# Kernel optimization log

Measured on AMD Instinct MI355X. Metric: run time of the kernel, lower is better.

The kernel has to match this reference:

```python
import jax, jax.numpy as jnp
import numpy as np

N, D, C, K = 16384, 128, 10, 16
EPS = float(np.finfo(np.float32).eps)
LOG2PI = float(np.log(2.0 * np.pi))


def setup_inputs() -> dict:
    key = jax.random.key(0)
    ks = jax.random.split(key, 8)
    X = jax.random.normal(ks[0], (N, D), dtype=jnp.float32)
    y = jax.random.randint(ks[1], (N,), 0, C, dtype=jnp.int32)
    responsibilities = jax.random.uniform(ks[2], (C, N, K), dtype=jnp.float32)
    mu = jax.random.normal(ks[3], (C, K, D), dtype=jnp.float32)
    # lower < mu < upper so the truncation normalizer is positive (as after gmm_initialisation)
    lower = mu - 1.0 + 0.1 * jax.random.normal(ks[4], (C, K, D), dtype=jnp.float32)
    upper = mu + 1.0 + 0.1 * jax.random.normal(ks[5], (C, K, D), dtype=jnp.float32)
    sigma = jnp.abs(jax.random.normal(ks[6], (C, K, D), dtype=jnp.float32))
    logits_k = jax.random.normal(ks[7], (C, K), dtype=jnp.float32)
    eta = jnp.float32(0.0)  # model initializes eta = 0.0 (non-trainable)
    return {"X": X, "y": y, "responsibilities": responsibilities, "mu": mu,
            "lower": lower, "upper": upper, "sigma": sigma,
            "logits_k": logits_k, "eta": eta}


def _stgma_loss(X, y, responsibilities, mu, lower, upper, sigma, logits_k, eta):
    # scale = eps + softplus(sigma), shape [C, K, D]
    scale = EPS + jax.nn.softplus(sigma)
    # normalizing constant per (class, component): prod_d [Phi(up) - Phi(lo)] + eps
    ndtr = jax.scipy.special.ndtr
    z = ndtr((upper - mu) / scale) - ndtr((lower - mu) / scale)       # [C, K, D]
    log_norm = jnp.log(jnp.prod(z, axis=-1) + EPS)                    # [C, K]
    log_cat = jax.nn.log_softmax(logits_k, axis=-1)                   # [C, K]

    # gather per-sample class parameters: [N, K, D]
    mu_y, lo_y, up_y, sc_y = mu[y], lower[y], upper[y], scale[y]
    xk = X[:, None, :]                                                # [N, 1, D]

    # soft truncation margins: sum_d -softplus(-eta * (x - lower)) etc.
    lp_low = -jnp.sum(jax.nn.softplus(-eta * (xk - lo_y)), axis=-1)   # [N, K]
    lp_up = -jnp.sum(jax.nn.softplus(-eta * (up_y - xk)), axis=-1)    # [N, K]

    # independent diagonal Normal log prob per component
    zd = (xk - mu_y) / sc_y
    comp_lp = jnp.sum(-0.5 * zd * zd - jnp.log(sc_y), axis=-1) - 0.5 * D * LOG2PI  # [N, K]

    log_pdf = log_cat[y] - log_norm[y] + lp_low + lp_up + comp_lp     # [N, K]

    # responsibilities for each sample from its own class
    resp = responsibilities[y, jnp.arange(N)]                         # [N, K]
    weighted = resp * log_pdf                                         # [N, K]

    # per-class reduce_mean over the class's samples and components, then -sum
    onehot = (y[:, None] == jnp.arange(C)[None, :]).astype(weighted.dtype)  # [N, C]
    class_sums = jnp.einsum('nk,nc->c', weighted, onehot)             # [C]
    counts = jnp.sum(onehot, axis=0) * K                              # [C]
    return -jnp.sum(class_sums / counts)


def reference(X, y, responsibilities, mu, lower, upper, sigma, logits_k, eta):
    return _stgma_loss(X, y, responsibilities, mu, lower, upper, sigma, logits_k, eta)
```

## Files before the change

kernel.cpp:

```cpp
#include <hip/hip_runtime.h>
#include <math.h>

#define N_PTS 16384
#define D_DIM 128
#define C_CLS 10
#define K_MIX 16

constexpr float EPSF   = 1.1920928955078125e-07f;
constexpr float LOG2PI = 1.8378770664093453f;
constexpr float LN2F   = 0.6931471805599453f;

__device__ __forceinline__ float softplusf(float x) {
    if (x > 20.f)  return x;
    if (x < -20.f) return expf(x);
    return log1pf(expf(x));
}
__device__ __forceinline__ float ndtrf(float x) {
    return 0.5f * erfcf(-x * 0.70710678118654752440f);
}

__global__ __launch_bounds__(64) void k_params(
    const float* __restrict__ mu, const float* __restrict__ lower,
    const float* __restrict__ upper, const float* __restrict__ sigma,
    float* __restrict__ muT, float* __restrict__ isT,
    float* __restrict__ loT, float* __restrict__ upT,
    float* __restrict__ Ack) {
    int b = blockIdx.x;
    int c = b / K_MIX, k = b % K_MIX;
    int lane = threadIdx.x;
    float ls_sum = 0.f;
    float zprod  = 1.f;
    #pragma unroll
    for (int half = 0; half < 2; ++half) {
        int d  = lane + 64 * half;
        int gi = (c * K_MIX + k) * D_DIM + d;
        float m  = mu[gi], lo = lower[gi], up = upper[gi], sg = sigma[gi];
        float sc = EPSF + softplusf(sg);
        float is = 1.f / sc;
        int ti = c * (D_DIM * K_MIX) + d * K_MIX + k;
        muT[ti] = m; isT[ti] = is; loT[ti] = lo; upT[ti] = up;
        ls_sum += logf(sc);
        float z = ndtrf((up - m) * is) - ndtrf((lo - m) * is);
        zprod *= z;
    }
    #pragma unroll
    for (int off = 1; off < 64; off <<= 1) {
        ls_sum += __shfl_xor(ls_sum, off);
        zprod  *= __shfl_xor(zprod, off);
    }
    if (lane == 0) {
        float log_norm = logf(zprod + EPSF);
        Ack[b] = -log_norm - ls_sum - 0.5f * (float)D_DIM * LOG2PI;
    }
}

__global__ __launch_bounds__(256) void k_const(
    const float* __restrict__ logits, const int* __restrict__ y,
    const float* __restrict__ Ack,
    float* __restrict__ const_ck, int* __restrict__ counts) {
    __shared__ int hist[C_CLS];
    int t = threadIdx.x;
    if (t < C_CLS) hist[t] = 0;
    __syncthreads();
    for (int i = t; i < N_PTS; i += 256) atomicAdd(&hist[y[i]], 1);
    __syncthreads();
    if (t < C_CLS) {
        int c = t;
        counts[c] = hist[c];
        float mx = -1e30f;
        for (int k = 0; k < K_MIX; ++k) mx = fmaxf(mx, logits[c * K_MIX + k]);
        float se = 0.f;
        for (int k = 0; k < K_MIX; ++k) se += expf(logits[c * K_MIX + k] - mx);
        float lse = mx + logf(se);
        for (int k = 0; k < K_MIX; ++k)
            const_ck[c * K_MIX + k] = logits[c * K_MIX + k] - lse + Ack[c * K_MIX + k];
    }
}

__global__ __launch_bounds__(256) void k_main(
    const float* __restrict__ X, const int* __restrict__ y,
    const float* __restrict__ resp,
    const float* __restrict__ muT, const float* __restrict__ isT,
    const float* __restrict__ loT, const float* __restrict__ upT,
    const float* __restrict__ const_ck, const int* __restrict__ counts,
    const float* __restrict__ etap, float* __restrict__ blockPartials) {
    __shared__ float xs[16][132];
    __shared__ float sums[16];
    int t  = threadIdx.x;
    int n0 = blockIdx.x * 16;

    #pragma unroll
    for (int i = 0; i < 2; ++i) {
        int j  = t * 2 + i;
        int r  = j >> 5, c4 = j & 31;
        float4 v = *reinterpret_cast<const float4*>(X + (size_t)(n0 + r) * D_DIM + c4 * 4);
        xs[r][c4 * 4 + 0] = v.x; xs[r][c4 * 4 + 1] = v.y;
        xs[r][c4 * 4 + 2] = v.z; xs[r][c4 * 4 + 3] = v.w;
    }
    __syncthreads();

    int k  = t & 15;
    int nl = (t >> 4) & 3;
    int w  = t >> 6;
    int n_local = w * 4 + nl;
    int n  = n0 + n_local;
    int c  = y[n];

    const float* mp = muT + (size_t)c * (D_DIM * K_MIX) + k;
    const float* sp = isT + (size_t)c * (D_DIM * K_MIX) + k;

    float acc = 0.f;
    #pragma unroll 4
    for (int d = 0; d < D_DIM; ++d) {
        float x  = xs[n_local][d];
        float zd = (x - mp[d * K_MIX]) * sp[d * K_MIX];
        acc = fmaf(zd, zd, acc);
    }

    float eta = etap[0];
    float lp;
    if (eta == 0.f) {
        lp = -2.f * (float)D_DIM * LN2F;
    } else {
        lp = 0.f;
        const float* lo = loT + (size_t)c * (D_DIM * K_MIX) + k;
        const float* up = upT + (size_t)c * (D_DIM * K_MIX) + k;
        for (int d = 0; d < D_DIM; ++d) {
            float x = xs[n_local][d];
            lp -= softplusf(-eta * (x - lo[d * K_MIX]))
                + softplusf(-eta * (up[d * K_MIX] - x));
        }
    }

    float r_ = resp[((size_t)c * N_PTS + n) * K_MIX + k];
    float v  = r_ * (const_ck[c * K_MIX + k] + lp - 0.5f * acc);
    v *= 1.f / ((float)counts[c] * (float)K_MIX);

    v += __shfl_xor(v, 1);
    v += __shfl_xor(v, 2);
    v += __shfl_xor(v, 4);
    v += __shfl_xor(v, 8);
    if (k == 0) sums[n_local] = v;
    __syncthreads();
    if (t == 0) {
        float s = 0.f;
        #pragma unroll
        for (int i = 0; i < 16; ++i) s += sums[i];
        blockPartials[blockIdx.x] = s;
    }
}

__global__ __launch_bounds__(256) void k_final(
    const float* __restrict__ blockPartials, float* __restrict__ out) {
    __shared__ float red[256];
    int t = threadIdx.x;
    float s = 0.f;
    for (int i = t; i < 1024; i += 256) s += blockPartials[i];
    red[t] = s;
    __syncthreads();
    for (int off = 128; off > 0; off >>= 1) {
        if (t < off) red[t] += red[t + off];
        __syncthreads();
    }
    if (t == 0) out[0] = -red[0];
}

extern "C" void kernel_launch(void* const* d_in, const int* in_sizes, int n_in,
                              void* d_out, int out_size, void* d_ws, size_t ws_size,
                              hipStream_t stream) {
    const float* X      = (const float*)d_in[0];
    const int*   y      = (const int*)  d_in[1];
    const float* resp   = (const float*)d_in[2];
    const float* mu     = (const float*)d_in[3];
    const float* lower  = (const float*)d_in[4];
    const float* upper  = (const float*)d_in[5];
    const float* sigma  = (const float*)d_in[6];
    const float* logits = (const float*)d_in[7];
    const float* eta    = (const float*)d_in[8];
    float* out = (float*)d_out;

    char* ws = (char*)d_ws;
    size_t off = 0;
    auto alloc = [&](size_t bytes) {
        void* p = ws + off;
        off += (bytes + 255) & ~size_t(255);
        return p;
    };
    const size_t PARAM = (size_t)C_CLS * D_DIM * K_MIX * sizeof(float);
    float* muT      = (float*)alloc(PARAM);
    float* isT      = (float*)alloc(PARAM);
    float* loT      = (float*)alloc(PARAM);
    float* upT      = (float*)alloc(PARAM);
    float* Ack      = (float*)alloc(C_CLS * K_MIX * sizeof(float));
    float* const_ck = (float*)alloc(C_CLS * K_MIX * sizeof(float));
    int*   counts   = (int*)  alloc(C_CLS * sizeof(int));
    float* partials = (float*)alloc((N_PTS / 16) * sizeof(float));

    k_params<<<C_CLS * K_MIX, 64, 0, stream>>>(mu, lower, upper, sigma,
                                               muT, isT, loT, upT, Ack);
    k_const<<<1, 256, 0, stream>>>(logits, y, Ack, const_ck, counts);
    k_main<<<N_PTS / 16, 256, 0, stream>>>(X, y, resp, muT, isT, loT, upT,
                                           const_ck, counts, eta, partials);
    k_final<<<1, 256, 0, stream>>>(partials, out);
}
```

Baseline: 35.02 us.

## Sort samples by class and keep per-class parameters in registers

```diff
diff --git a/kernel.cpp b/kernel.cpp
--- a/kernel.cpp
+++ b/kernel.cpp
@@ -5,6 +5,8 @@
 #define D_DIM 128
 #define C_CLS 10
 #define K_MIX 16
+#define HIST_BLOCKS 64
+#define MAIN_BPC 32
 
 constexpr float EPSF   = 1.1920928955078125e-07f;
 constexpr float LOG2PI = 1.8378770664093453f;
@@ -19,143 +21,205 @@
     return 0.5f * erfcf(-x * 0.70710678118654752440f);
 }
 
-__global__ __launch_bounds__(64) void k_params(
+__global__ __launch_bounds__(256) void k_prep(
     const float* __restrict__ mu, const float* __restrict__ lower,
     const float* __restrict__ upper, const float* __restrict__ sigma,
-    float* __restrict__ muT, float* __restrict__ isT,
-    float* __restrict__ loT, float* __restrict__ upT,
-    float* __restrict__ Ack) {
+    const int* __restrict__ y,
+    float2* __restrict__ abT, float* __restrict__ loT, float* __restrict__ upT,
+    float* __restrict__ Ack, int* __restrict__ blockCnt) {
+    int b = blockIdx.x, t = threadIdx.x;
+    if (b < C_CLS * K_MIX) {
+        int c = b / K_MIX, k = b % K_MIX;
+        __shared__ float rs0[256], rs1[256], rp[256];
+        float logsc = 0.f, mu2 = 0.f, zz = 1.f;
+        if (t < D_DIM) {
+            int gi = b * D_DIM + t;
+            float m = mu[gi], lo = lower[gi], up = upper[gi], sg = sigma[gi];
+            float sc = EPSF + softplusf(sg);
+            float is = 1.f / sc;
+            int ti = (c * D_DIM + t) * K_MIX + k;
+            abT[ti] = make_float2(is * is, 2.f * m * is * is);
+            loT[ti] = lo; upT[ti] = up;
+            logsc = logf(sc);
+            mu2   = m * m * is * is;
+            zz    = ndtrf((up - m) * is) - ndtrf((lo - m) * is);
+        }
+        rs0[t] = logsc; rs1[t] = mu2; rp[t] = zz;
+        __syncthreads();
+        for (int off = 128; off > 0; off >>= 1) {
+            if (t < off) { rs0[t] += rs0[t+off]; rs1[t] += rs1[t+off]; rp[t] *= rp[t+off]; }
+            __syncthreads();
+        }
+        if (t == 0) {
+            float log_norm = logf(rp[0] + EPSF);
+            Ack[b] = -log_norm - rs0[0] - 0.5f * (float)D_DIM * LOG2PI - 0.5f * rs1[0];
+        }
+    } else {
+        int h = b - C_CLS * K_MIX;
+        __shared__ int hist[C_CLS];
+        if (t < C_CLS) hist[t] = 0;
+        __syncthreads();
+        int c = y[h * 256 + t];
+        int lane = t & 63;
+        for (int cc = 0; cc < C_CLS; ++cc) {
+            unsigned long long m = __ballot(c == cc);
+            if (lane == 0 && m) atomicAdd(&hist[cc], __popcll(m));
+        }
+        __syncthreads();
+        if (t < C_CLS) blockCnt[h * C_CLS + t] = hist[t];
+    }
+}
+
+__global__ __launch_bounds__(256) void k_scatter(
+    const int* __restrict__ y, const int* __restrict__ blockCnt,
+    const float* __restrict__ logits, const float* __restrict__ Ack,
+    int* __restrict__ idxSorted, int* __restrict__ classOff,
+    float* __restrict__ invden, float* __restrict__ const_ck) {
+    __shared__ int sCnt[HIST_BLOCKS * C_CLS];
+    __shared__ int sClassOff[C_CLS + 1];
+    __shared__ int myOff[C_CLS];
+    __shared__ int wcnt[4][C_CLS];
+    __shared__ int wbase[4][C_CLS];
+    int h = blockIdx.x, t = threadIdx.x;
+    for (int i = t; i < HIST_BLOCKS * C_CLS; i += 256) sCnt[i] = blockCnt[i];
+    __syncthreads();
+    if (t == 0) {
+        int acc = 0;
+        for (int c = 0; c < C_CLS; ++c) {
+            sClassOff[c] = acc;
+            int s = 0;
+            for (int hh = 0; hh < HIST_BLOCKS; ++hh) s += sCnt[hh * C_CLS + c];
+            acc += s;
+        }
+        sClassOff[C_CLS] = acc;
+    }
+    __syncthreads();
+    if (t < C_CLS) {
+        int s = sClassOff[t];
+        for (int hh = 0; hh < h; ++hh) s += sCnt[hh * C_CLS + t];
+        myOff[t] = s;
+    }
+    __syncthreads();
+    int n = h * 256 + t;
+    int c = y[n];
+    int w = t >> 6, lane = t & 63;
+    int rank = 0;
+    for (int cc = 0; cc < C_CLS; ++cc) {
+        unsigned long long m = __ballot(c == cc);
+        if (c == cc) rank = __popcll(m & ((1ull << lane) - 1ull));
+        if (lane == 0) wcnt[w][cc] = __popcll(m);
+    }
+    __syncthreads();
+    if (t < 4 * C_CLS) {
+        int ww = t / C_CLS, cc = t % C_CLS;
+        int s = myOff[cc];
+        for (int w2 = 0; w2 < ww; ++w2) s += wcnt[w2][cc];
+        wbase[ww][cc] = s;
+    }
+    __syncthreads();
+    idxSorted[wbase[w][c] + rank] = n;
+
+    if (h == 0) {
+        __shared__ float lse[C_CLS];
+        if (t < C_CLS) {
+            float mx = -1e30f;
+            for (int k = 0; k < K_MIX; ++k) mx = fmaxf(mx, logits[t * K_MIX + k]);
+            float se = 0.f;
+            for (int k = 0; k < K_MIX; ++k) se += expf(logits[t * K_MIX + k] - mx);
+            lse[t] = mx + logf(se);
+            int cnt = sClassOff[t + 1] - sClassOff[t];
+            invden[t] = (cnt > 0) ? 1.f / ((float)cnt * (float)K_MIX) : 0.f;
+        }
+        if (t < C_CLS + 1) classOff[t] = sClassOff[t];
+        __syncthreads();
+        if (t < C_CLS * K_MIX) const_ck[t] = logits[t] - lse[t / K_MIX] + Ack[t];
+    }
+}
+
+__global__ __launch_bounds__(256) void k_main(
+    const float* __restrict__ X, const float* __restrict__ resp,
+    const float2* __restrict__ abT, const float* __restrict__ loT,
+    const float* __restrict__ upT, const float* __restrict__ const_ck,
+    const int* __restrict__ classOff, const float* __restrict__ invden,
+    const int* __restrict__ idxSorted, const float* __restrict__ etap,
+    float* __restrict__ partials) {
     int b = blockIdx.x;
-    int c = b / K_MIX, k = b % K_MIX;
-    int lane = threadIdx.x;
-    float ls_sum = 0.f;
-    float zprod  = 1.f;
+    int c = b / MAIN_BPC, j = b % MAIN_BPC;
+    int t = threadIdx.x;
+    int w = t >> 6, lane = t & 63;
+    int k = lane & 15, dc = lane >> 4;
+    const int d0 = dc * 32;
+
+    float a_[32], b_[32];
+    const float2* ab = abT + (size_t)c * D_DIM * K_MIX + k;
     #pragma unroll
-    for (int half = 0; half < 2; ++half) {
-        int d  = lane + 64 * half;
-        int gi = (c * K_MIX + k) * D_DIM + d;
-        float m  = mu[gi], lo = lower[gi], up = upper[gi], sg = sigma[gi];
-        float sc = EPSF + softplusf(sg);
-        float is = 1.f / sc;
-        int ti = c * (D_DIM * K_MIX) + d * K_MIX + k;
-        muT[ti] = m; isT[ti] = is; loT[ti] = lo; upT[ti] = up;
-        ls_sum += logf(sc);
-        float z = ndtrf((up - m) * is) - ndtrf((lo - m) * is);
-        zprod *= z;
-    }
-    #pragma unroll
-    for (int off = 1; off < 64; off <<= 1) {
-        ls_sum += __shfl_xor(ls_sum, off);
-        zprod  *= __shfl_xor(zprod, off);
-    }
-    if (lane == 0) {
-        float log_norm = logf(zprod + EPSF);
-        Ack[b] = -log_norm - ls_sum - 0.5f * (float)D_DIM * LOG2PI;
-    }
-}
-
-__global__ __launch_bounds__(256) void k_const(
-    const float* __restrict__ logits, const int* __restrict__ y,
-    const float* __restrict__ Ack,
-    float* __restrict__ const_ck, int* __restrict__ counts) {
-    __shared__ int hist[C_CLS];
-    int t = threadIdx.x;
-    if (t < C_CLS) hist[t] = 0;
-    __syncthreads();
-    for (int i = t; i < N_PTS; i += 256) atomicAdd(&hist[y[i]], 1);
-    __syncthreads();
-    if (t < C_CLS) {
-        int c = t;
-        counts[c] = hist[c];
-        float mx = -1e30f;
-        for (int k = 0; k < K_MIX; ++k) mx = fmaxf(mx, logits[c * K_MIX + k]);
-        float se = 0.f;
-        for (int k = 0; k < K_MIX; ++k) se += expf(logits[c * K_MIX + k] - mx);
-        float lse = mx + logf(se);
-        for (int k = 0; k < K_MIX; ++k)
-            const_ck[c * K_MIX + k] = logits[c * K_MIX + k] - lse + Ack[c * K_MIX + k];
-    }
-}
-
-__global__ __launch_bounds__(256) void k_main(
-    const float* __restrict__ X, const int* __restrict__ y,
-    const float* __restrict__ resp,
-    const float* __restrict__ muT, const float* __restrict__ isT,
-    const float* __restrict__ loT, const float* __restrict__ upT,
-    const float* __restrict__ const_ck, const int* __restrict__ counts,
-    const float* __restrict__ etap, float* __restrict__ blockPartials) {
-    __shared__ float xs[16][132];
-    __shared__ float sums[16];
-    int t  = threadIdx.x;
-    int n0 = blockIdx.x * 16;
-
-    #pragma unroll
-    for (int i = 0; i < 2; ++i) {
-        int j  = t * 2 + i;
-        int r  = j >> 5, c4 = j & 31;
-        float4 v = *reinterpret_cast<const float4*>(X + (size_t)(n0 + r) * D_DIM + c4 * 4);
-        xs[r][c4 * 4 + 0] = v.x; xs[r][c4 * 4 + 1] = v.y;
-        xs[r][c4 * 4 + 2] = v.z; xs[r][c4 * 4 + 3] = v.w;
-    }
-    __syncthreads();
-
-    int k  = t & 15;
-    int nl = (t >> 4) & 3;
-    int w  = t >> 6;
-    int n_local = w * 4 + nl;
-    int n  = n0 + n_local;
-    int c  = y[n];
-
-    const float* mp = muT + (size_t)c * (D_DIM * K_MIX) + k;
-    const float* sp = isT + (size_t)c * (D_DIM * K_MIX) + k;
-
-    float acc = 0.f;
-    #pragma unroll 4
-    for (int d = 0; d < D_DIM; ++d) {
-        float x  = xs[n_local][d];
-        float zd = (x - mp[d * K_MIX]) * sp[d * K_MIX];
-        acc = fmaf(zd, zd, acc);
-    }
-
+    for (int i = 0; i < 32; ++i) {
+        float2 v = ab[(size_t)(d0 + i) * K_MIX];
+        a_[i] = v.x; b_[i] = v.y;
+    }
+    float ck  = const_ck[c * K_MIX + k];
     float eta = etap[0];
-    float lp;
-    if (eta == 0.f) {
-        lp = -2.f * (float)D_DIM * LN2F;
-    } else {
-        lp = 0.f;
-        const float* lo = loT + (size_t)c * (D_DIM * K_MIX) + k;
-        const float* up = upT + (size_t)c * (D_DIM * K_MIX) + k;
-        for (int d = 0; d < D_DIM; ++d) {
-            float x = xs[n_local][d];
-            lp -= softplusf(-eta * (x - lo[d * K_MIX]))
-                + softplusf(-eta * (up[d * K_MIX] - x));
-        }
-    }
-
-    float r_ = resp[((size_t)c * N_PTS + n) * K_MIX + k];
-    float v  = r_ * (const_ck[c * K_MIX + k] + lp - 0.5f * acc);
-    v *= 1.f / ((float)counts[c] * (float)K_MIX);
-
-    v += __shfl_xor(v, 1);
-    v += __shfl_xor(v, 2);
-    v += __shfl_xor(v, 4);
-    v += __shfl_xor(v, 8);
-    if (k == 0) sums[n_local] = v;
-    __syncthreads();
-    if (t == 0) {
-        float s = 0.f;
-        #pragma unroll
-        for (int i = 0; i < 16; ++i) s += sums[i];
-        blockPartials[blockIdx.x] = s;
-    }
+    float inv = invden[c];
+    int off = classOff[c];
+    int cnt = classOff[c + 1] - off;
+    const float lpconst = -2.f * (float)D_DIM * LN2F;
+
+    float wsum = 0.f;
+    for (int p = j * 4 + w; p < cnt; p += MAIN_BPC * 4) {
+        int n = idxSorted[off + p];
+        const float* xr = X + (size_t)n * D_DIM + d0;
+        float acc = 0.f, lp = lpconst;
+        if (eta == 0.f) {
+            #pragma unroll
+            for (int i4 = 0; i4 < 8; ++i4) {
+                float4 xv = *reinterpret_cast<const float4*>(xr + i4 * 4);
+                acc = fmaf(xv.x, fmaf(a_[i4*4+0], xv.x, -b_[i4*4+0]), acc);
+                acc = fmaf(xv.y, fmaf(a_[i4*4+1], xv.y, -b_[i4*4+1]), acc);
+                acc = fmaf(xv.z, fmaf(a_[i4*4+2], xv.z, -b_[i4*4+2]), acc);
+                acc = fmaf(xv.w, fmaf(a_[i4*4+3], xv.w, -b_[i4*4+3]), acc);
+            }
+            acc += __shfl_xor(acc, 16);
+            acc += __shfl_xor(acc, 32);
+        } else {
+            float lpp = 0.f;
+            const float* lo = loT + (size_t)c * D_DIM * K_MIX + k;
+            const float* up = upT + (size_t)c * D_DIM * K_MIX + k;
+            #pragma unroll
+            for (int i4 = 0; i4 < 8; ++i4) {
+                float4 xv = *reinterpret_cast<const float4*>(xr + i4 * 4);
+                float xs4[4] = {xv.x, xv.y, xv.z, xv.w};
+                #pragma unroll
+                for (int q = 0; q < 4; ++q) {
+                    int i = i4 * 4 + q;
+                    float x = xs4[q];
+                    acc = fmaf(x, fmaf(a_[i], x, -b_[i]), acc);
+                    float lov = lo[(size_t)(d0 + i) * K_MIX];
+                    float upv = up[(size_t)(d0 + i) * K_MIX];
+                    lpp -= softplusf(-eta * (x - lov)) + softplusf(-eta * (upv - x));
+                }
+            }
+            acc += __shfl_xor(acc, 16); acc += __shfl_xor(acc, 32);
+            lpp += __shfl_xor(lpp, 16); lpp += __shfl_xor(lpp, 32);
+            lp = lpp;
+        }
+        float r = resp[((size_t)c * N_PTS + n) * K_MIX + k];
+        float v = r * (ck + lp - 0.5f * acc) * inv;
+        v += __shfl_xor(v, 1); v += __shfl_xor(v, 2);
+        v += __shfl_xor(v, 4); v += __shfl_xor(v, 8);
+        wsum += v;
+    }
+    __shared__ float ws[4];
+    if (lane == 0) ws[w] = wsum;
+    __syncthreads();
+    if (t == 0) partials[b] = ws[0] + ws[1] + ws[2] + ws[3];
 }
 
 __global__ __launch_bounds__(256) void k_final(
-    const float* __restrict__ blockPartials, float* __restrict__ out) {
+    const float* __restrict__ partials, float* __restrict__ out) {
     __shared__ float red[256];
     int t = threadIdx.x;
     float s = 0.f;
-    for (int i = t; i < 1024; i += 256) s += blockPartials[i];
+    for (int i = t; i < C_CLS * MAIN_BPC; i += 256) s += partials[i];
     red[t] = s;
     __syncthreads();
     for (int off = 128; off > 0; off >>= 1) {
@@ -186,20 +250,23 @@
         off += (bytes + 255) & ~size_t(255);
         return p;
     };
-    const size_t PARAM = (size_t)C_CLS * D_DIM * K_MIX * sizeof(float);
-    float* muT      = (float*)alloc(PARAM);
-    float* isT      = (float*)alloc(PARAM);
-    float* loT      = (float*)alloc(PARAM);
-    float* upT      = (float*)alloc(PARAM);
-    float* Ack      = (float*)alloc(C_CLS * K_MIX * sizeof(float));
-    float* const_ck = (float*)alloc(C_CLS * K_MIX * sizeof(float));
-    int*   counts   = (int*)  alloc(C_CLS * sizeof(int));
-    float* partials = (float*)alloc((N_PTS / 16) * sizeof(float));
-
-    k_params<<<C_CLS * K_MIX, 64, 0, stream>>>(mu, lower, upper, sigma,
-                                               muT, isT, loT, upT, Ack);
-    k_const<<<1, 256, 0, stream>>>(logits, y, Ack, const_ck, counts);
-    k_main<<<N_PTS / 16, 256, 0, stream>>>(X, y, resp, muT, isT, loT, upT,
-                                           const_ck, counts, eta, partials);
+    const size_t PE = (size_t)C_CLS * D_DIM * K_MIX;
+    float2* abT      = (float2*)alloc(PE * sizeof(float2));
+    float*  loT      = (float*) alloc(PE * sizeof(float));
+    float*  upT      = (float*) alloc(PE * sizeof(float));
+    float*  Ack      = (float*) alloc(C_CLS * K_MIX * sizeof(float));
+    float*  const_ck = (float*) alloc(C_CLS * K_MIX * sizeof(float));
+    int*    blockCnt = (int*)   alloc(HIST_BLOCKS * C_CLS * sizeof(int));
+    int*    idxSorted= (int*)   alloc(N_PTS * sizeof(int));
+    int*    classOff = (int*)   alloc((C_CLS + 1) * sizeof(int));
+    float*  invden   = (float*) alloc(C_CLS * sizeof(float));
+    float*  partials = (float*) alloc(C_CLS * MAIN_BPC * sizeof(float));
+
+    k_prep<<<C_CLS * K_MIX + HIST_BLOCKS, 256, 0, stream>>>(
+        mu, lower, upper, sigma, y, abT, loT, upT, Ack, blockCnt);
+    k_scatter<<<HIST_BLOCKS, 256, 0, stream>>>(
+        y, blockCnt, logits, Ack, idxSorted, classOff, invden, const_ck);
+    k_main<<<C_CLS * MAIN_BPC, 256, 0, stream>>>(
+        X, resp, abT, loT, upT, const_ck, classOff, invden, idxSorted, eta, partials);
     k_final<<<1, 256, 0, stream>>>(partials, out);
 }
```

New measurement: 34.53 us. About the same (-1.4%).

## Fuse param prep into class-partitioned main kernel with register-resident expanded quadratic

Applied to the files above, without the earlier changes.

```diff
diff --git a/kernel.cpp b/kernel.cpp
--- a/kernel.cpp
+++ b/kernel.cpp
@@ -5,6 +5,9 @@
 #define D_DIM 128
 #define C_CLS 10
 #define K_MIX 16
+#define BPC   51
+#define GRID  (C_CLS * BPC)
+#define NCHUNK (N_PTS / 64)
 
 constexpr float EPSF   = 1.1920928955078125e-07f;
 constexpr float LOG2PI = 1.8378770664093453f;
@@ -19,150 +22,189 @@
     return 0.5f * erfcf(-x * 0.70710678118654752440f);
 }
 
-__global__ __launch_bounds__(64) void k_params(
+__global__ __launch_bounds__(256, 2) void k_main(
+    const float* __restrict__ X, const int* __restrict__ y,
+    const float* __restrict__ resp,
     const float* __restrict__ mu, const float* __restrict__ lower,
     const float* __restrict__ upper, const float* __restrict__ sigma,
-    float* __restrict__ muT, float* __restrict__ isT,
-    float* __restrict__ loT, float* __restrict__ upT,
-    float* __restrict__ Ack) {
-    int b = blockIdx.x;
-    int c = b / K_MIX, k = b % K_MIX;
-    int lane = threadIdx.x;
-    float ls_sum = 0.f;
-    float zprod  = 1.f;
+    const float* __restrict__ etap,
+    float* __restrict__ Ack, float* __restrict__ partials1,
+    float* __restrict__ partials2, int* __restrict__ countB) {
+    const int b = blockIdx.x, t = threadIdx.x;
+    const int w = t >> 6, lane = t & 63;
+    const int c = b / BPC, j = b % BPC;
+    const int k = lane & 15, dc = lane >> 4;
+    const int d0 = dc * 32;
+
+    __shared__ float zW[4][16];
+    __shared__ float sWsum[4];
+    __shared__ float sRk[4][16];
+    __shared__ int   sCntW[4];
+
+    const size_t pbase = ((size_t)(c * K_MIX + k)) * D_DIM + d0;
+    float a_[32], b_[32];
+    float logsc = 0.f, mu2 = 0.f;
     #pragma unroll
-    for (int half = 0; half < 2; ++half) {
-        int d  = lane + 64 * half;
-        int gi = (c * K_MIX + k) * D_DIM + d;
-        float m  = mu[gi], lo = lower[gi], up = upper[gi], sg = sigma[gi];
-        float sc = EPSF + softplusf(sg);
-        float is = 1.f / sc;
-        int ti = c * (D_DIM * K_MIX) + d * K_MIX + k;
-        muT[ti] = m; isT[ti] = is; loT[ti] = lo; upT[ti] = up;
-        ls_sum += logf(sc);
-        float z = ndtrf((up - m) * is) - ndtrf((lo - m) * is);
-        zprod *= z;
-    }
-    #pragma unroll
-    for (int off = 1; off < 64; off <<= 1) {
-        ls_sum += __shfl_xor(ls_sum, off);
-        zprod  *= __shfl_xor(zprod, off);
-    }
-    if (lane == 0) {
-        float log_norm = logf(zprod + EPSF);
-        Ack[b] = -log_norm - ls_sum - 0.5f * (float)D_DIM * LOG2PI;
-    }
-}
-
-__global__ __launch_bounds__(256) void k_const(
-    const float* __restrict__ logits, const int* __restrict__ y,
-    const float* __restrict__ Ack,
-    float* __restrict__ const_ck, int* __restrict__ counts) {
-    __shared__ int hist[C_CLS];
-    int t = threadIdx.x;
-    if (t < C_CLS) hist[t] = 0;
-    __syncthreads();
-    for (int i = t; i < N_PTS; i += 256) atomicAdd(&hist[y[i]], 1);
-    __syncthreads();
-    if (t < C_CLS) {
-        int c = t;
-        counts[c] = hist[c];
-        float mx = -1e30f;
-        for (int k = 0; k < K_MIX; ++k) mx = fmaxf(mx, logits[c * K_MIX + k]);
-        float se = 0.f;
-        for (int k = 0; k < K_MIX; ++k) se += expf(logits[c * K_MIX + k] - mx);
-        float lse = mx + logf(se);
-        for (int k = 0; k < K_MIX; ++k)
-            const_ck[c * K_MIX + k] = logits[c * K_MIX + k] - lse + Ack[c * K_MIX + k];
-    }
-}
-
-__global__ __launch_bounds__(256) void k_main(
-    const float* __restrict__ X, const int* __restrict__ y,
-    const float* __restrict__ resp,
-    const float* __restrict__ muT, const float* __restrict__ isT,
-    const float* __restrict__ loT, const float* __restrict__ upT,
-    const float* __restrict__ const_ck, const int* __restrict__ counts,
-    const float* __restrict__ etap, float* __restrict__ blockPartials) {
-    __shared__ float xs[16][132];
-    __shared__ float sums[16];
-    int t  = threadIdx.x;
-    int n0 = blockIdx.x * 16;
-
-    #pragma unroll
-    for (int i = 0; i < 2; ++i) {
-        int j  = t * 2 + i;
-        int r  = j >> 5, c4 = j & 31;
-        float4 v = *reinterpret_cast<const float4*>(X + (size_t)(n0 + r) * D_DIM + c4 * 4);
-        xs[r][c4 * 4 + 0] = v.x; xs[r][c4 * 4 + 1] = v.y;
-        xs[r][c4 * 4 + 2] = v.z; xs[r][c4 * 4 + 3] = v.w;
-    }
-    __syncthreads();
-
-    int k  = t & 15;
-    int nl = (t >> 4) & 3;
-    int w  = t >> 6;
-    int n_local = w * 4 + nl;
-    int n  = n0 + n_local;
-    int c  = y[n];
-
-    const float* mp = muT + (size_t)c * (D_DIM * K_MIX) + k;
-    const float* sp = isT + (size_t)c * (D_DIM * K_MIX) + k;
-
-    float acc = 0.f;
-    #pragma unroll 4
-    for (int d = 0; d < D_DIM; ++d) {
-        float x  = xs[n_local][d];
-        float zd = (x - mp[d * K_MIX]) * sp[d * K_MIX];
-        acc = fmaf(zd, zd, acc);
-    }
-
-    float eta = etap[0];
-    float lp;
-    if (eta == 0.f) {
-        lp = -2.f * (float)D_DIM * LN2F;
-    } else {
-        lp = 0.f;
-        const float* lo = loT + (size_t)c * (D_DIM * K_MIX) + k;
-        const float* up = upT + (size_t)c * (D_DIM * K_MIX) + k;
-        for (int d = 0; d < D_DIM; ++d) {
-            float x = xs[n_local][d];
-            lp -= softplusf(-eta * (x - lo[d * K_MIX]))
-                + softplusf(-eta * (up[d * K_MIX] - x));
-        }
-    }
-
-    float r_ = resp[((size_t)c * N_PTS + n) * K_MIX + k];
-    float v  = r_ * (const_ck[c * K_MIX + k] + lp - 0.5f * acc);
-    v *= 1.f / ((float)counts[c] * (float)K_MIX);
-
-    v += __shfl_xor(v, 1);
-    v += __shfl_xor(v, 2);
-    v += __shfl_xor(v, 4);
-    v += __shfl_xor(v, 8);
-    if (k == 0) sums[n_local] = v;
+    for (int i4 = 0; i4 < 8; ++i4) {
+        float4 mv = *reinterpret_cast<const float4*>(mu    + pbase + i4 * 4);
+        float4 sv = *reinterpret_cast<const float4*>(sigma + pbase + i4 * 4);
+        float m4[4] = {mv.x, mv.y, mv.z, mv.w};
+        float s4[4] = {sv.x, sv.y, sv.z, sv.w};
+        #pragma unroll
+        for (int q = 0; q < 4; ++q) {
+            int i = i4 * 4 + q;
+            float sc = EPSF + softplusf(s4[q]);
+            float is = 1.f / sc;
+            a_[i] = is * is;
+            b_[i] = 2.f * m4[q] * is * is;
+            logsc += logf(sc);
+            mu2   += m4[q] * m4[q] * is * is;
+        }
+    }
+
+    if (j == 0) {
+        float zp = 1.f;
+        const size_t zbase = pbase + w * 8;
+        #pragma unroll
+        for (int i4 = 0; i4 < 2; ++i4) {
+            float4 mv = *reinterpret_cast<const float4*>(mu    + zbase + i4 * 4);
+            float4 sv = *reinterpret_cast<const float4*>(sigma + zbase + i4 * 4);
+            float4 lv = *reinterpret_cast<const float4*>(lower + zbase + i4 * 4);
+            float4 uv = *reinterpret_cast<const float4*>(upper + zbase + i4 * 4);
+            float m4[4] = {mv.x, mv.y, mv.z, mv.w};
+            float s4[4] = {sv.x, sv.y, sv.z, sv.w};
+            float l4[4] = {lv.x, lv.y, lv.z, lv.w};
+            float u4[4] = {uv.x, uv.y, uv.z, uv.w};
+            #pragma unroll
+            for (int q = 0; q < 4; ++q) {
+                float sc = EPSF + softplusf(s4[q]);
+                float is = 1.f / sc;
+                zp *= ndtrf((u4[q] - m4[q]) * is) - ndtrf((l4[q] - m4[q]) * is);
+            }
+        }
+        zp *= __shfl_xor(zp, 16);
+        zp *= __shfl_xor(zp, 32);
+        if (lane < 16) zW[w][lane] = zp;
+    }
+    float logscF = logsc + 0.f, mu2F = mu2 + 0.f;
+    logscF += __shfl_xor(logscF, 16); logscF += __shfl_xor(logscF, 32);
+    mu2F   += __shfl_xor(mu2F, 16);   mu2F   += __shfl_xor(mu2F, 32);
+    if (j == 0) {
+        __syncthreads();
+        if (w == 0 && lane < 16) {
+            float zp = zW[0][lane] * zW[1][lane] * zW[2][lane] * zW[3][lane];
+            Ack[c * K_MIX + lane] = -logf(zp + EPSF) - logscF
+                                  - 0.5f * (float)D_DIM * LOG2PI - 0.5f * mu2F;
+        }
+    }
+
+    const float eta = etap[0];
+    const float lpconst = -2.f * (float)D_DIM * LN2F;
+    float wsum = 0.f, rk = 0.f;
+    int myCount = 0;
+
+    for (int q = j * 4 + w; q < NCHUNK; q += BPC * 4) {
+        int n0 = q * 64;
+        int yv = y[n0 + lane];
+        unsigned long long m = __ballot(yv == c);
+        myCount += __popcll(m);
+        while (m) {
+            int s = __builtin_ctzll(m);
+            m &= m - 1;
+            int n = n0 + s;
+            const float* xr = X + (size_t)n * D_DIM + d0;
+            float acc = 0.f, lp = lpconst;
+            #pragma unroll
+            for (int i4 = 0; i4 < 8; ++i4) {
+                float4 xv = *reinterpret_cast<const float4*>(xr + i4 * 4);
+                acc = fmaf(xv.x, fmaf(a_[i4*4+0], xv.x, -b_[i4*4+0]), acc);
+                acc = fmaf(xv.y, fmaf(a_[i4*4+1], xv.y, -b_[i4*4+1]), acc);
+                acc = fmaf(xv.z, fmaf(a_[i4*4+2], xv.z, -b_[i4*4+2]), acc);
+                acc = fmaf(xv.w, fmaf(a_[i4*4+3], xv.w, -b_[i4*4+3]), acc);
+            }
+            if (eta != 0.f) {
+                float lpp = 0.f;
+                #pragma unroll
+                for (int i4 = 0; i4 < 8; ++i4) {
+                    float4 xv = *reinterpret_cast<const float4*>(xr + i4 * 4);
+                    float4 lv = *reinterpret_cast<const float4*>(lower + pbase + i4 * 4);
+                    float4 uv = *reinterpret_cast<const float4*>(upper + pbase + i4 * 4);
+                    float x4[4] = {xv.x, xv.y, xv.z, xv.w};
+                    float l4[4] = {lv.x, lv.y, lv.z, lv.w};
+                    float u4[4] = {uv.x, uv.y, uv.z, uv.w};
+                    #pragma unroll
+                    for (int qq = 0; qq < 4; ++qq)
+                        lpp -= softplusf(-eta * (x4[qq] - l4[qq]))
+                             + softplusf(-eta * (u4[qq] - x4[qq]));
+                }
+                lpp += __shfl_xor(lpp, 16);
+                lpp += __shfl_xor(lpp, 32);
+                lp = lpp;
+            }
+            acc += __shfl_xor(acc, 16);
+            acc += __shfl_xor(acc, 32);
+            float r = resp[((size_t)c * N_PTS + n) * K_MIX + k];
+            rk += r;
+            float v = r * fmaf(-0.5f, acc, lp);
+            v += __shfl_xor(v, 1); v += __shfl_xor(v, 2);
+            v += __shfl_xor(v, 4); v += __shfl_xor(v, 8);
+            wsum += v;
+        }
+    }
+
+    if (lane == 0) { sWsum[w] = wsum; sCntW[w] = myCount; }
+    if (lane < 16) sRk[w][lane] = rk;
     __syncthreads();
     if (t == 0) {
+        partials1[b] = sWsum[0] + sWsum[1] + sWsum[2] + sWsum[3];
+        countB[b]    = sCntW[0] + sCntW[1] + sCntW[2] + sCntW[3];
+    }
+    if (t < K_MIX)
+        partials2[b * K_MIX + t] = sRk[0][t] + sRk[1][t] + sRk[2][t] + sRk[3][t];
+}
+
+__global__ __launch_bounds__(256) void k_final(
+    const float* __restrict__ logits, const float* __restrict__ Ack,
+    const float* __restrict__ partials1, const float* __restrict__ partials2,
+    const int* __restrict__ countB, float* __restrict__ out) {
+    __shared__ float sS1[C_CLS];
+    __shared__ int   sCnt[C_CLS];
+    __shared__ float sLse[C_CLS];
+    __shared__ float sR[C_CLS * K_MIX];
+    int t = threadIdx.x;
+    if (t < C_CLS) {
+        float s = 0.f; int cn = 0;
+        for (int jj = 0; jj < BPC; ++jj) {
+            s  += partials1[t * BPC + jj];
+            cn += countB[t * BPC + jj];
+        }
+        sS1[t] = s; sCnt[t] = cn;
+        float mx = -1e30f;
+        for (int k = 0; k < K_MIX; ++k) mx = fmaxf(mx, logits[t * K_MIX + k]);
+        float se = 0.f;
+        for (int k = 0; k < K_MIX; ++k) se += expf(logits[t * K_MIX + k] - mx);
+        sLse[t] = mx + logf(se);
+    }
+    if (t < C_CLS * K_MIX) {
+        int c = t / K_MIX, k = t % K_MIX;
         float s = 0.f;
-        #pragma unroll
-        for (int i = 0; i < 16; ++i) s += sums[i];
-        blockPartials[blockIdx.x] = s;
-    }
-}
-
-__global__ __launch_bounds__(256) void k_final(
-    const float* __restrict__ blockPartials, float* __restrict__ out) {
-    __shared__ float red[256];
-    int t = threadIdx.x;
-    float s = 0.f;
-    for (int i = t; i < 1024; i += 256) s += blockPartials[i];
-    red[t] = s;
+        for (int jj = 0; jj < BPC; ++jj)
+            s += partials2[((size_t)(c * BPC + jj)) * K_MIX + k];
+        sR[t] = s;
+    }
     __syncthreads();
-    for (int off = 128; off > 0; off >>= 1) {
-        if (t < off) red[t] += red[t + off];
-        __syncthreads();
-    }
-    if (t == 0) out[0] = -red[0];
+    if (t == 0) {
+        float loss = 0.f;
+        for (int c = 0; c < C_CLS; ++c) {
+            float cs = sS1[c];
+            for (int k = 0; k < K_MIX; ++k)
+                cs += sR[c * K_MIX + k]
+                    * (logits[c * K_MIX + k] - sLse[c] + Ack[c * K_MIX + k]);
+            float den = (float)sCnt[c] * (float)K_MIX;
+            if (sCnt[c] > 0) loss += cs / den;
+        }
+        out[0] = -loss;
+    }
 }
 
 extern "C" void kernel_launch(void* const* d_in, const int* in_sizes, int n_in,
@@ -186,20 +228,12 @@
         off += (bytes + 255) & ~size_t(255);
         return p;
     };
-    const size_t PARAM = (size_t)C_CLS * D_DIM * K_MIX * sizeof(float);
-    float* muT      = (float*)alloc(PARAM);
-    float* isT      = (float*)alloc(PARAM);
-    float* loT      = (float*)alloc(PARAM);
-    float* upT      = (float*)alloc(PARAM);
-    float* Ack      = (float*)alloc(C_CLS * K_MIX * sizeof(float));
-    float* const_ck = (float*)alloc(C_CLS * K_MIX * sizeof(float));
-    int*   counts   = (int*)  alloc(C_CLS * sizeof(int));
-    float* partials = (float*)alloc((N_PTS / 16) * sizeof(float));
-
-    k_params<<<C_CLS * K_MIX, 64, 0, stream>>>(mu, lower, upper, sigma,
-                                               muT, isT, loT, upT, Ack);
-    k_const<<<1, 256, 0, stream>>>(logits, y, Ack, const_ck, counts);
-    k_main<<<N_PTS / 16, 256, 0, stream>>>(X, y, resp, muT, isT, loT, upT,
-                                           const_ck, counts, eta, partials);
-    k_final<<<1, 256, 0, stream>>>(partials, out);
-}
+    float* Ack       = (float*)alloc(C_CLS * K_MIX * sizeof(float));
+    float* partials1 = (float*)alloc(GRID * sizeof(float));
+    float* partials2 = (float*)alloc(GRID * K_MIX * sizeof(float));
+    int*   countB    = (int*)  alloc(GRID * sizeof(int));
+
+    k_main<<<GRID, 256, 0, stream>>>(X, y, resp, mu, lower, upper, sigma, eta,
+                                     Ack, partials1, partials2, countB);
+    k_final<<<1, 256, 0, stream>>>(logits, Ack, partials1, partials2, countB, out);
+}
```

Result: slower. 48.32 us (+38.0%).
